# Kernel optimization log

Hardware: AMD Instinct MI355X
Metric: run time of the kernel (lower is better)

Reference implementation:

```python
import jax, jax.numpy as jnp
import numpy as np

N = 1024       # sentence length (words incl. root at index 0)
WD = 300       # word embedding dim (GloVe-style)
PD = 25        # pos_emb_dim
H = 125        # hidden_dim_lstm
FC = 100       # hidden_dim_fc
PVOCAB = 50    # POS tagset size


def setup_inputs() -> dict:
    key = jax.random.key(0)
    ks = jax.random.split(key, 14)
    f = lambda k, s: jax.random.normal(k, s, dtype=jnp.float32) * 0.1
    d_in = WD + PD
    return {
        "word_vecs": jax.random.normal(ks[0], (N, WD), dtype=jnp.float32),
        "pos_idx": jax.random.randint(ks[1], (N,), 0, PVOCAB),
        "parents_ids": jax.random.randint(ks[2], (N,), 0, N),
        "pos_emb": f(ks[3], (PVOCAB, PD)),
        "Wih0": f(ks[4], (2, 4 * H, d_in)),
        "Whh0": f(ks[5], (2, 4 * H, H)),
        "b0": f(ks[6], (2, 4 * H)),
        "Wih1": f(ks[7], (2, 4 * H, 2 * H)),
        "Whh1": f(ks[8], (2, 4 * H, H)),
        "b1": f(ks[9], (2, 4 * H)),
        "fc1_W": f(ks[10], (FC, 4 * H)),
        "fc1_b": f(ks[11], (FC,)),
        "fc2_W": f(ks[12], (1, FC)),
        "fc2_b": f(ks[13], (1,)),
    }


def _lstm_dir(x, Wih, Whh, b, reverse):
    # torch LSTM cell, gate order (i, f, g, o); b = b_ih + b_hh
    Hd = Whh.shape[1]
    def step(carry, xt):
        h, c = carry
        g = xt @ Wih.T + h @ Whh.T + b
        i, fg, gg, o = jnp.split(g, 4)
        i = jax.nn.sigmoid(i)
        fg = jax.nn.sigmoid(fg)
        gg = jnp.tanh(gg)
        o = jax.nn.sigmoid(o)
        c = fg * c + i * gg
        h = o * jnp.tanh(c)
        return (h, c), h
    init = (jnp.zeros((Hd,), x.dtype), jnp.zeros((Hd,), x.dtype))
    _, hs = jax.lax.scan(step, init, x, reverse=reverse)
    return hs  # [n, H], already in original time order


def _bilstm_layer(x, Wih, Whh, b):
    hf = _lstm_dir(x, Wih[0], Whh[0], b[0], False)
    hb = _lstm_dir(x, Wih[1], Whh[1], b[1], True)
    return jnp.concatenate([hf, hb], axis=1)  # [n, 2H]


def reference(word_vecs, pos_idx, parents_ids, pos_emb, Wih0, Whh0, b0,
              Wih1, Whh1, b1, fc1_W, fc1_b, fc2_W, fc2_b):
    # encoder: concat word + pos embeddings, 2-layer BiLSTM
    x = jnp.concatenate([word_vecs, pos_emb[pos_idx]], axis=1)  # [n, WD+PD]
    h = _bilstm_layer(x, Wih0, Whh0, b0)
    h = _bilstm_layer(h, Wih1, Whh1, b1)  # [n, 2H]
    n = h.shape[0]
    twoH = h.shape[1]
    # fc1(cat(h_i, h_j)) = h_i @ W_head^T + h_j @ W_child^T + b  (vectorized over all pairs)
    A = h @ fc1_W[:, :twoH].T   # head contribution  [n, FC]
    B = h @ fc1_W[:, twoH:].T   # child contribution [n, FC]
    T = jnp.tanh(A[:, None, :] + B[None, :, :] + fc1_b)  # [n, n, FC]
    raw = T @ fc2_W[0] + fc2_b[0]                         # [n, n]
    ii = jnp.arange(n)
    # original loop skips diagonal and arcs into the root (j == 0); those stay 0
    mask = (ii[:, None] != ii[None, :]) & (ii[None, :] != 0)
    scores_mat = jnp.where(mask, raw, jnp.float32(0.0))
    logits = scores_mat.T  # row j = scores of heads for child j
    logp = jax.nn.log_softmax(logits, axis=1)
    loss = -jnp.mean(logp[jnp.arange(n), parents_ids])
    return loss, scores_mat
```

## Files before the change

kernel.cpp:

```cpp
#include <hip/hip_runtime.h>

typedef float v2f __attribute__((ext_vector_type(2)));
typedef float v4f __attribute__((ext_vector_type(4)));

#define LOG2E 1.4426950408889634f
#define LN2   0.6931471805599453f

__device__ __forceinline__ float fexp2(float x) {
  float r; asm("v_exp_f32 %0, %1" : "=v"(r) : "v"(x)); return r;
}
__device__ __forceinline__ float frcp(float x) {
  float r; asm("v_rcp_f32 %0, %1" : "=v"(r) : "v"(x)); return r;
}
__device__ __forceinline__ float flog2(float x) {
  float r; asm("v_log_f32 %0, %1" : "=v"(r) : "v"(x)); return r;
}
__device__ __forceinline__ v2f pkfma(v2f a, v2f b, v2f c) {
  v2f d; asm("v_pk_fma_f32 %0, %1, %2, %3" : "=v"(d) : "v"(a), "v"(b), "v"(c));
  return d;
}
__device__ __forceinline__ float dpp_xor1(float v) {
  return __builtin_bit_cast(float,
      __builtin_amdgcn_update_dpp(0, __builtin_bit_cast(int, v), 0xB1, 0xF, 0xF, true));
}
__device__ __forceinline__ float dpp_xor2(float v) {
  return __builtin_bit_cast(float,
      __builtin_amdgcn_update_dpp(0, __builtin_bit_cast(int, v), 0x4E, 0xF, 0xF, true));
}
__device__ __forceinline__ void barrier_lgkm() {
  asm volatile("s_waitcnt lgkmcnt(0)\n\ts_barrier" ::: "memory");
}

__global__ void k_embed(const float* __restrict__ wv, const int* __restrict__ pidx,
                        const float* __restrict__ pemb, float* __restrict__ X) {
  int t = blockIdx.x;
  int pi = pidx[t];
  for (int c = threadIdx.x; c < 336; c += 128) {
    float v;
    if (c < 300)      v = wv[t * 300 + c];
    else if (c < 325) v = pemb[pi * 25 + (c - 300)];
    else              v = 0.f;
    X[t * 336 + c] = v;
  }
}

__global__ void k_repack(const float* __restrict__ src, float* __restrict__ dst,
                         int sK, int dK, int doScale) {
  int r = blockIdx.x;
  float sc = 1.f;
  if (doScale) { int gate = (r % 500) / 125; sc = (gate == 2) ? 2.f * LOG2E : LOG2E; }
  for (int c = threadIdx.x; c < dK; c += 128)
    dst[r * dK + c] = (c < sK) ? src[r * sK + c] * sc : 0.f;
}

__global__ void k_bscale(const float* __restrict__ b, float* __restrict__ bs) {
  int i = blockIdx.x * 256 + threadIdx.x;
  if (i < 1000) {
    int gate = (i % 500) / 125;
    bs[i] = b[i] * ((gate == 2) ? 2.f * LOG2E : LOG2E);
  }
}

__global__ void k_wab(const float* __restrict__ fc1W, float* __restrict__ Wab) {
  int r = blockIdx.x;
  int sr = (r < 100) ? r : r - 100;
  int so = (r < 100) ? 0 : 250;
  for (int c = threadIdx.x; c < 256; c += 128)
    Wab[r * 256 + c] = (c < 250) ? fc1W[sr * 500 + so + c] : 0.f;
}

__global__ void k_misc(const float* __restrict__ fc1b, const float* __restrict__ fc2W,
                       float* __restrict__ biasAB, float* __restrict__ sumw) {
  __shared__ float red[128];
  int t = threadIdx.x;
  for (int c = t; c < 256; c += 128)
    biasAB[c] = (c < 100) ? fc1b[c] : 0.f;
  float s = (t < 100) ? fc2W[t] : 0.f;
  red[t] = s; __syncthreads();
  for (int off = 64; off; off >>= 1) {
    if (t < off) red[t] += red[t + off];
    __syncthreads();
  }
  if (t == 0) sumw[0] = red[0];
}

#define BM 64
#define BN 64
#define BKK 16
__global__ __launch_bounds__(256) void k_gemm(
    const float* __restrict__ A, const float* __restrict__ Bw,
    const float* __restrict__ bias, float* __restrict__ C,
    int M, int N, int K, int ldC, long sBz, long sCz, long sbz, int transOut) {
  const int z = blockIdx.z;
  const float* Bp = Bw + (size_t)z * sBz;
  const float* bp = bias + (size_t)z * sbz;
  float* Cp = C + (size_t)z * sCz;
  const int bm = blockIdx.y * BM, bn = blockIdx.x * BN;
  __shared__ __align__(16) float As[BKK][BM + 4];
  __shared__ __align__(16) float Bs[BKK][BN + 4];
  __shared__ float Ts[BN][BM + 1];
  const int tid = threadIdx.x;
  const int tx = tid & 15, ty = tid >> 4;
  const int lr = tid >> 2;
  const int lk = (tid & 3) * 4;
  float acc[4][4];
#pragma unroll
  for (int a = 0; a < 4; ++a)
#pragma unroll
    for (int b = 0; b < 4; ++b) acc[a][b] = 0.f;

  int brow = bn + lr; if (brow >= N) brow = N - 1;
  for (int k0 = 0; k0 < K; k0 += BKK) {
    float4 a4 = *(const float4*)(A + (size_t)(bm + lr) * K + k0 + lk);
    float4 b4 = *(const float4*)(Bp + (size_t)brow * K + k0 + lk);
    __syncthreads();
    As[lk + 0][lr] = a4.x; As[lk + 1][lr] = a4.y; As[lk + 2][lr] = a4.z; As[lk + 3][lr] = a4.w;
    Bs[lk + 0][lr] = b4.x; Bs[lk + 1][lr] = b4.y; Bs[lk + 2][lr] = b4.z; Bs[lk + 3][lr] = b4.w;
    __syncthreads();
#pragma unroll
    for (int kk = 0; kk < BKK; ++kk) {
      float4 av = *(const float4*)&As[kk][ty * 4];
      float4 bv = *(const float4*)&Bs[kk][tx * 4];
      float aa[4] = {av.x, av.y, av.z, av.w};
      float bb[4] = {bv.x, bv.y, bv.z, bv.w};
#pragma unroll
      for (int a = 0; a < 4; ++a)
#pragma unroll
        for (int b = 0; b < 4; ++b)
          acc[a][b] = __builtin_fmaf(aa[a], bb[b], acc[a][b]);
    }
  }
  if (!transOut) {
#pragma unroll
    for (int a = 0; a < 4; ++a) {
      int i = bm + ty * 4 + a;
#pragma unroll
      for (int b = 0; b < 4; ++b) {
        int j = bn + tx * 4 + b;
        if (j < N) Cp[(size_t)i * ldC + j] = acc[a][b] + bp[j];
      }
    }
  } else {
    __syncthreads();
#pragma unroll
    for (int a = 0; a < 4; ++a)
#pragma unroll
      for (int b = 0; b < 4; ++b) {
        int jn = bn + tx * 4 + b; if (jn >= N) jn = N - 1;
        Ts[tx * 4 + b][ty * 4 + a] = acc[a][b] + bp[jn];
      }
    __syncthreads();
    const int n2 = tid >> 2, mq = (tid & 3) * 16;
    const int n = bn + n2;
    if (n < N) {
#pragma unroll
      for (int r = 0; r < 4; ++r) {
        int m0 = mq + r * 4;
        float4 v;
        v.x = Ts[n2][m0 + 0]; v.y = Ts[n2][m0 + 1];
        v.z = Ts[n2][m0 + 2]; v.w = Ts[n2][m0 + 3];
        *(float4*)(Cp + (size_t)n * ldC + bm + m0) = v;
      }
    }
  }
}

template<bool FWD>
__device__ __forceinline__ void rec_loop(
    const float4* __restrict__ Pr, const v2f (&w)[4][16],
    float (*hb)[160], float (*hist)[128],
    float* __restrict__ hout, int d, int t, int u, int sub, bool active,
    float sA, float sB) {
  const bool b1s = (sub & 1) != 0;
  const bool b2s = (sub & 2) != 0;
  const bool wr = (sub == 0) && active;
  float cst = 0.f;
  float4 cura = Pr[FWD ? 0 : 254];
  float4 curb = Pr[FWD ? 1 : 255];
  barrier_lgkm();

  for (int cb = 0; cb < 128; ++cb) {
    int nc = (cb + 1 < 128) ? cb + 1 : cb;
    float4 nxta = Pr[FWD ? 2 * nc     : 254 - 2 * nc];
    float4 nxtb = Pr[FWD ? 2 * nc + 1 : 255 - 2 * nc];
#pragma unroll
    for (int e = 0; e < 8; ++e) {
      const int buf = e & 1;
      float pre;
      if (FWD)
        pre = (e == 0) ? cura.x : (e == 1) ? cura.y : (e == 2) ? cura.z : (e == 3) ? cura.w
            : (e == 4) ? curb.x : (e == 5) ? curb.y : (e == 6) ? curb.z : curb.w;
      else
        pre = (e == 0) ? curb.w : (e == 1) ? curb.z : (e == 2) ? curb.y : (e == 3) ? curb.x
            : (e == 4) ? cura.w : (e == 5) ? cura.z : (e == 6) ? cura.y : cura.x;
      const v4f* hp = (const v4f*)&hb[buf][36 * sub];
      v2f a0 = {0.f, 0.f}, a1 = {0.f, 0.f}, a2 = {0.f, 0.f}, a3 = {0.f, 0.f};
#pragma unroll
      for (int q = 0; q < 8; ++q) {
        v4f hv = hp[q];
        v2f ha = __builtin_shufflevector(hv, hv, 0, 1);
        v2f hc = __builtin_shufflevector(hv, hv, 2, 3);
        a0 = pkfma(w[0][2 * q], ha, a0); a0 = pkfma(w[0][2 * q + 1], hc, a0);
        a1 = pkfma(w[1][2 * q], ha, a1); a1 = pkfma(w[1][2 * q + 1], hc, a1);
        a2 = pkfma(w[2][2 * q], ha, a2); a2 = pkfma(w[2][2 * q + 1], hc, a2);
        a3 = pkfma(w[3][2 * q], ha, a3); a3 = pkfma(w[3][2 * q + 1], hc, a3);
      }
      float p0 = a0.x + a0.y, p1 = a1.x + a1.y, p2 = a2.x + a2.y, p3 = a3.x + a3.y;
      float s01 = b1s ? p0 : p1, k01 = b1s ? p1 : p0;
      float r01 = k01 + dpp_xor1(s01);
      float s23 = b1s ? p2 : p3, k23 = b1s ? p3 : p2;
      float r23 = k23 + dpp_xor1(s23);
      float sv = b2s ? r01 : r23, kv = b2s ? r23 : r01;
      float x = kv + dpp_xor2(sv) + pre;
      float sg = frcp(1.f + fexp2(-x));
      float a = __builtin_fmaf(sA, sg, sB);
      float fg = dpp_xor1(a);
      float gg = dpp_xor2(a);
      float og = dpp_xor2(fg);
      cst = __builtin_fmaf(fg, cst, a * gg);
      float th = __builtin_fmaf(2.f, frcp(1.f + fexp2(-2.f * LOG2E * cst)), -1.f);
      float h = og * th;
      if (wr) {
        hb[buf ^ 1][u + 4 * (u >> 5)] = h;
        hist[(cb & 3) * 8 + e][u] = h;
      }
      barrier_lgkm();
    }
    if ((cb & 3) == 3) {
      const int S0 = (cb - 3) * 8;
#pragma unroll
      for (int k = 0; k < 8; ++k) {
        int idx = t + k * 512;
        int r = idx >> 7, u2 = idx & 127;
        if (u2 < 125) {
          int step = S0 + r;
          int time = FWD ? step : 1023 - step;
          hout[(size_t)time * 256 + d * 125 + u2] = hist[r][u2];
        }
      }
      barrier_lgkm();
    }
    cura = nxta; curb = nxtb;
  }
}

__global__ __launch_bounds__(512, 2) void k_rec(const float* __restrict__ Pt,
                                                const float* __restrict__ Whh,
                                                float* __restrict__ hout) {
  const int d = blockIdx.x;
  const int t = threadIdx.x;
  int u = t >> 2; const bool active = (u < 125); if (u > 124) u = 124;
  const int sub = t & 3;

  const float* Wd = Whh + (size_t)d * 500 * 125;
  v2f w[4][16];
#pragma unroll
  for (int g = 0; g < 4; ++g) {
    const float sc = (g == 2) ? 2.f * LOG2E : LOG2E;
    const float* wrp = Wd + (size_t)(g * 125 + u) * 125;
#pragma unroll
    for (int j = 0; j < 16; ++j) {
      int col = sub * 32 + 2 * j;
      v2f ww;
      ww.x = (col     < 125) ? wrp[col]     * sc : 0.f;
      ww.y = (col + 1 < 125) ? wrp[col + 1] * sc : 0.f;
      w[g][j] = ww;
    }
  }

  __shared__ __align__(16) float hb[2][160];
  __shared__ float hist[32][128];
  for (int i = t; i < 320; i += 512) ((float*)hb)[i] = 0.f;

  const int prow = sub * 125 + u;
  const float4* Pr = (const float4*)(Pt + (size_t)d * 500 * 1024 + (size_t)prow * 1024);
  const float sA = (sub == 2) ? 2.f : 1.f;
  const float sB = (sub == 2) ? -1.f : 0.f;

  if (d == 0) rec_loop<true >(Pr, w, hb, hist, hout, d, t, u, sub, active, sA, sB);
  else        rec_loop<false>(Pr, w, hb, hist, hout, d, t, u, sub, active, sA, sB);
}

__global__ __launch_bounds__(256) void k_pair(const float* __restrict__ AB,
    const float* __restrict__ fc2W, const float* __restrict__ fc2b,
    const float* __restrict__ sumw, float* __restrict__ outS,
    float* __restrict__ scoresT) {
  __shared__ float As[32][100];
  __shared__ float Bs[32][101];
  __shared__ float w2s[100];
  const int tid = threadIdx.x;
  const int i0 = blockIdx.y * 32, j0 = blockIdx.x * 32;
  for (int idx = tid; idx < 3200; idx += 256) {
    int r = idx / 100, k = idx - r * 100;
    As[r][k] = AB[(size_t)(i0 + r) * 200 + k];
    Bs[r][k] = AB[(size_t)(j0 + r) * 200 + 100 + k];
  }
  if (tid < 100) w2s[tid] = 2.f * fc2W[tid];
  __syncthreads();
  const int tx = tid & 31, ty = tid >> 5;
  float acc[4] = {0.f, 0.f, 0.f, 0.f};
#pragma unroll 4
  for (int k = 0; k < 100; ++k) {
    float b = Bs[tx][k];
    float wk2 = w2s[k];
    float bs = b * (2.f * LOG2E);
#pragma unroll
    for (int q = 0; q < 4; ++q) {
      float a = As[ty + 8 * q][k];
      float r = frcp(1.f + fexp2(__builtin_fmaf(a, 2.f * LOG2E, bs)));
      acc[q] = __builtin_fmaf(wk2, r, acc[q]);
    }
  }
  float base = sumw[0] + fc2b[0];
  const int j = j0 + tx;
#pragma unroll
  for (int q = 0; q < 4; ++q) {
    int i = i0 + ty + 8 * q;
    float val = (i != j && j != 0) ? (base - acc[q]) : 0.f;
    outS[(size_t)i * 1024 + j] = val;
    scoresT[(size_t)j * 1024 + i] = val;
  }
}

__global__ __launch_bounds__(256) void k_soft(const float* __restrict__ scoresT,
    const int* __restrict__ parents, float* __restrict__ contrib) {
  const int j = blockIdx.x, tid = threadIdx.x;
  __shared__ float red[256];
  const float* row = scoresT + (size_t)j * 1024;
  float v0 = row[tid], v1 = row[tid + 256], v2 = row[tid + 512], v3 = row[tid + 768];
  float m = fmaxf(fmaxf(v0, v1), fmaxf(v2, v3));
  red[tid] = m; __syncthreads();
  for (int off = 128; off; off >>= 1) {
    if (tid < off) red[tid] = fmaxf(red[tid], red[tid + off]);
    __syncthreads();
  }
  m = red[0]; __syncthreads();
  float s = fexp2((v0 - m) * LOG2E) + fexp2((v1 - m) * LOG2E) +
            fexp2((v2 - m) * LOG2E) + fexp2((v3 - m) * LOG2E);
  red[tid] = s; __syncthreads();
  for (int off = 128; off; off >>= 1) {
    if (tid < off) red[tid] += red[tid + off];
    __syncthreads();
  }
  if (tid == 0) {
    float S = red[0];
    int p = parents[j];
    contrib[j] = row[p] - m - flog2(S) * LN2;
  }
}

__global__ __launch_bounds__(256) void k_loss(const float* __restrict__ contrib,
                                              float* __restrict__ out) {
  __shared__ float red[256];
  int tid = threadIdx.x;
  float s = contrib[tid] + contrib[tid + 256] + contrib[tid + 512] + contrib[tid + 768];
  red[tid] = s; __syncthreads();
  for (int off = 128; off; off >>= 1) {
    if (tid < off) red[tid] += red[tid + off];
    __syncthreads();
  }
  if (tid == 0) out[0] = -red[0] * (1.f / 1024.f);
}

extern "C" void kernel_launch(void* const* d_in, const int* in_sizes, int n_in,
                              void* d_out, int out_size, void* d_ws, size_t ws_size,
                              hipStream_t stream) {
  const float* wv   = (const float*)d_in[0];
  const int*   pidx = (const int*)d_in[1];
  const int*   par  = (const int*)d_in[2];
  const float* pemb = (const float*)d_in[3];
  const float* Wih0 = (const float*)d_in[4];
  const float* Whh0 = (const float*)d_in[5];
  const float* b0   = (const float*)d_in[6];
  const float* Wih1 = (const float*)d_in[7];
  const float* Whh1 = (const float*)d_in[8];
  const float* b1   = (const float*)d_in[9];
  const float* fc1W = (const float*)d_in[10];
  const float* fc1b = (const float*)d_in[11];
  const float* fc2W = (const float*)d_in[12];
  const float* fc2b = (const float*)d_in[13];
  float* ws = (float*)d_ws;
  float* X      = ws + 0;
  float* Wih0p  = ws + 344064;
  float* Pt0    = ws + 680064;
  float* h0     = ws + 1704064;
  float* Wih1p  = ws + 1966208;
  float* Pt1    = ws + 2222208;
  float* h1     = ws + 3246208;
  float* Wab    = ws + 3508352;
  float* biasAB = ws + 3559552;
  float* AB     = ws + 3559808;
  float* scT    = ws + 3764608;
  float* contrib= ws + 4813184;
  float* sumw   = ws + 4814208;
  float* bs0    = ws + 4814212;
  float* bs1    = ws + 4815212;
  float* out = (float*)d_out;

  hipMemsetAsync(h0, 0, 1024 * 256 * sizeof(float), stream);
  hipMemsetAsync(h1, 0, 1024 * 256 * sizeof(float), stream);

  k_embed <<<1024, 128, 0, stream>>>(wv, pidx, pemb, X);
  k_repack<<<1000, 128, 0, stream>>>(Wih0, Wih0p, 325, 336, 1);
  k_repack<<<1000, 128, 0, stream>>>(Wih1, Wih1p, 250, 256, 1);
  k_bscale<<<4, 256, 0, stream>>>(b0, bs0);
  k_bscale<<<4, 256, 0, stream>>>(b1, bs1);
  k_wab   <<<200, 128, 0, stream>>>(fc1W, Wab);
  k_misc  <<<1, 128, 0, stream>>>(fc1b, fc2W, biasAB, sumw);

  k_gemm<<<dim3(8, 16, 2), 256, 0, stream>>>(X, Wih0p, bs0, Pt0, 1024, 500, 336, 1024,
                                             500L * 336, 500L * 1024, 500L, 1);
  k_rec <<<2, 512, 0, stream>>>(Pt0, Whh0, h0);
  k_gemm<<<dim3(8, 16, 2), 256, 0, stream>>>(h0, Wih1p, bs1, Pt1, 1024, 500, 256, 1024,
                                             500L * 256, 500L * 1024, 500L, 1);
  k_rec <<<2, 512, 0, stream>>>(Pt1, Whh1, h1);
  k_gemm<<<dim3(4, 16, 1), 256, 0, stream>>>(h1, Wab, biasAB, AB, 1024, 200, 256, 200,
                                             0L, 0L, 0L, 0);
  k_pair<<<dim3(32, 32), 256, 0, stream>>>(AB, fc2W, fc2b, sumw, out + 1, scT);
  k_soft<<<1024, 256, 0, stream>>>(scT, par, contrib);
  k_loss<<<1, 256, 0, stream>>>(contrib, out);
}
```

Measured before the change: 1.354 ms.

## Restructure LSTM recurrence to 2 threads per unit computing all four gates

The recurrent kernel now assigns each hidden unit to 2 lanes instead of 4. Each lane covers half of the hidden vector for all four gates, which replaces the gate-transposing DPP shuffles with a single xor1 reduction per gate. The input-projection scale is halved (the two lanes each add half of it), and the block shrinks to 256 threads, which removes one reduction level and the cross-lane gate exchange on the serial critical path. In exchange each lane does twice the FMAs and holds 256 weight registers, so register pressure and per-step compute latency go up.

```diff
diff --git a/kernel.cpp b/kernel.cpp
--- a/kernel.cpp
+++ b/kernel.cpp
@@ -15,17 +15,12 @@
 __device__ __forceinline__ float flog2(float x) {
   float r; asm("v_log_f32 %0, %1" : "=v"(r) : "v"(x)); return r;
 }
-__device__ __forceinline__ v2f pkfma(v2f a, v2f b, v2f c) {
-  v2f d; asm("v_pk_fma_f32 %0, %1, %2, %3" : "=v"(d) : "v"(a), "v"(b), "v"(c));
-  return d;
+__device__ __forceinline__ void pkfma(v2f& c, v2f a, v2f b) {
+  asm("v_pk_fma_f32 %0, %1, %2, %0" : "+v"(c) : "v"(a), "v"(b));
 }
 __device__ __forceinline__ float dpp_xor1(float v) {
   return __builtin_bit_cast(float,
       __builtin_amdgcn_update_dpp(0, __builtin_bit_cast(int, v), 0xB1, 0xF, 0xF, true));
-}
-__device__ __forceinline__ float dpp_xor2(float v) {
-  return __builtin_bit_cast(float,
-      __builtin_amdgcn_update_dpp(0, __builtin_bit_cast(int, v), 0x4E, 0xF, 0xF, true));
 }
 __device__ __forceinline__ void barrier_lgkm() {
   asm volatile("s_waitcnt lgkmcnt(0)\n\ts_barrier" ::: "memory");
@@ -48,7 +43,7 @@
                          int sK, int dK, int doScale) {
   int r = blockIdx.x;
   float sc = 1.f;
-  if (doScale) { int gate = (r % 500) / 125; sc = (gate == 2) ? 2.f * LOG2E : LOG2E; }
+  if (doScale) { int gate = (r % 500) / 125; sc = (gate == 2) ? LOG2E : 0.5f * LOG2E; }
   for (int c = threadIdx.x; c < dK; c += 128)
     dst[r * dK + c] = (c < sK) ? src[r * sK + c] * sc : 0.f;
 }
@@ -57,7 +52,7 @@
   int i = blockIdx.x * 256 + threadIdx.x;
   if (i < 1000) {
     int gate = (i % 500) / 125;
-    bs[i] = b[i] * ((gate == 2) ? 2.f * LOG2E : LOG2E);
+    bs[i] = b[i] * ((gate == 2) ? LOG2E : 0.5f * LOG2E);
   }
 }
 
@@ -165,72 +160,65 @@
   }
 }
 
+__device__ __forceinline__ float elem(float4 v, int e) {
+  return (e == 0) ? v.x : (e == 1) ? v.y : (e == 2) ? v.z : v.w;
+}
+
 template<bool FWD>
 __device__ __forceinline__ void rec_loop(
-    const float4* __restrict__ Pr, const v2f (&w)[4][16],
-    float (*hb)[160], float (*hist)[128],
-    float* __restrict__ hout, int d, int t, int u, int sub, bool active,
-    float sA, float sB) {
-  const bool b1s = (sub & 1) != 0;
-  const bool b2s = (sub & 2) != 0;
-  const bool wr = (sub == 0) && active;
+    const float4* __restrict__ P0, const float4* __restrict__ P1,
+    const float4* __restrict__ P2, const float4* __restrict__ P3,
+    const v2f (&w)[4][32], float (*hb)[128], float (*hist)[128],
+    float* __restrict__ hout, int d, int t, int u, int sub, bool wr) {
   float cst = 0.f;
-  float4 cura = Pr[FWD ? 0 : 254];
-  float4 curb = Pr[FWD ? 1 : 255];
+  float4 cur0 = P0[FWD ? 0 : 255], cur1 = P1[FWD ? 0 : 255];
+  float4 cur2 = P2[FWD ? 0 : 255], cur3 = P3[FWD ? 0 : 255];
   barrier_lgkm();
 
-  for (int cb = 0; cb < 128; ++cb) {
-    int nc = (cb + 1 < 128) ? cb + 1 : cb;
-    float4 nxta = Pr[FWD ? 2 * nc     : 254 - 2 * nc];
-    float4 nxtb = Pr[FWD ? 2 * nc + 1 : 255 - 2 * nc];
-#pragma unroll
-    for (int e = 0; e < 8; ++e) {
+  for (int cb = 0; cb < 256; ++cb) {
+    int nc = (cb + 1 < 256) ? cb + 1 : cb;
+    int ni = FWD ? nc : 255 - nc;
+    float4 nxt0 = P0[ni], nxt1 = P1[ni], nxt2 = P2[ni], nxt3 = P3[ni];
+#pragma unroll
+    for (int e = 0; e < 4; ++e) {
       const int buf = e & 1;
-      float pre;
-      if (FWD)
-        pre = (e == 0) ? cura.x : (e == 1) ? cura.y : (e == 2) ? cura.z : (e == 3) ? cura.w
-            : (e == 4) ? curb.x : (e == 5) ? curb.y : (e == 6) ? curb.z : curb.w;
-      else
-        pre = (e == 0) ? curb.w : (e == 1) ? curb.z : (e == 2) ? curb.y : (e == 3) ? curb.x
-            : (e == 4) ? cura.w : (e == 5) ? cura.z : (e == 6) ? cura.y : cura.x;
-      const v4f* hp = (const v4f*)&hb[buf][36 * sub];
+      const int ee = FWD ? e : 3 - e;
+      float pr0 = elem(cur0, ee), pr1 = elem(cur1, ee);
+      float pr2 = elem(cur2, ee), pr3 = elem(cur3, ee);
+      const v4f* hp = (const v4f*)&hb[buf][sub * 64];
       v2f a0 = {0.f, 0.f}, a1 = {0.f, 0.f}, a2 = {0.f, 0.f}, a3 = {0.f, 0.f};
 #pragma unroll
-      for (int q = 0; q < 8; ++q) {
+      for (int q = 0; q < 16; ++q) {
         v4f hv = hp[q];
         v2f ha = __builtin_shufflevector(hv, hv, 0, 1);
         v2f hc = __builtin_shufflevector(hv, hv, 2, 3);
-        a0 = pkfma(w[0][2 * q], ha, a0); a0 = pkfma(w[0][2 * q + 1], hc, a0);
-        a1 = pkfma(w[1][2 * q], ha, a1); a1 = pkfma(w[1][2 * q + 1], hc, a1);
-        a2 = pkfma(w[2][2 * q], ha, a2); a2 = pkfma(w[2][2 * q + 1], hc, a2);
-        a3 = pkfma(w[3][2 * q], ha, a3); a3 = pkfma(w[3][2 * q + 1], hc, a3);
-      }
-      float p0 = a0.x + a0.y, p1 = a1.x + a1.y, p2 = a2.x + a2.y, p3 = a3.x + a3.y;
-      float s01 = b1s ? p0 : p1, k01 = b1s ? p1 : p0;
-      float r01 = k01 + dpp_xor1(s01);
-      float s23 = b1s ? p2 : p3, k23 = b1s ? p3 : p2;
-      float r23 = k23 + dpp_xor1(s23);
-      float sv = b2s ? r01 : r23, kv = b2s ? r23 : r01;
-      float x = kv + dpp_xor2(sv) + pre;
-      float sg = frcp(1.f + fexp2(-x));
-      float a = __builtin_fmaf(sA, sg, sB);
-      float fg = dpp_xor1(a);
-      float gg = dpp_xor2(a);
-      float og = dpp_xor2(fg);
-      cst = __builtin_fmaf(fg, cst, a * gg);
+        pkfma(a0, w[0][2 * q], ha); pkfma(a0, w[0][2 * q + 1], hc);
+        pkfma(a1, w[1][2 * q], ha); pkfma(a1, w[1][2 * q + 1], hc);
+        pkfma(a2, w[2][2 * q], ha); pkfma(a2, w[2][2 * q + 1], hc);
+        pkfma(a3, w[3][2 * q], ha); pkfma(a3, w[3][2 * q + 1], hc);
+      }
+      float p0 = a0.x + a0.y + pr0;  p0 += dpp_xor1(p0);
+      float p1 = a1.x + a1.y + pr1;  p1 += dpp_xor1(p1);
+      float p2 = a2.x + a2.y + pr2;  p2 += dpp_xor1(p2);
+      float p3 = a3.x + a3.y + pr3;  p3 += dpp_xor1(p3);
+      float gi = frcp(1.f + fexp2(-p0));
+      float gf = frcp(1.f + fexp2(-p1));
+      float gg = __builtin_fmaf(2.f, frcp(1.f + fexp2(-p2)), -1.f);
+      float go = frcp(1.f + fexp2(-p3));
+      cst = __builtin_fmaf(gf, cst, gi * gg);
       float th = __builtin_fmaf(2.f, frcp(1.f + fexp2(-2.f * LOG2E * cst)), -1.f);
-      float h = og * th;
+      float h = go * th;
       if (wr) {
-        hb[buf ^ 1][u + 4 * (u >> 5)] = h;
-        hist[(cb & 3) * 8 + e][u] = h;
+        hb[buf ^ 1][u] = h;
+        hist[(cb & 7) * 4 + e][u] = h;
       }
       barrier_lgkm();
     }
-    if ((cb & 3) == 3) {
-      const int S0 = (cb - 3) * 8;
-#pragma unroll
-      for (int k = 0; k < 8; ++k) {
-        int idx = t + k * 512;
+    if ((cb & 7) == 7) {
+      const int S0 = 4 * cb - 28;
+#pragma unroll
+      for (int k = 0; k < 16; ++k) {
+        int idx = t + k * 256;
         int r = idx >> 7, u2 = idx & 127;
         if (u2 < 125) {
           int step = S0 + r;
@@ -240,27 +228,28 @@
       }
       barrier_lgkm();
     }
-    cura = nxta; curb = nxtb;
-  }
-}
-
-__global__ __launch_bounds__(512, 2) void k_rec(const float* __restrict__ Pt,
+    cur0 = nxt0; cur1 = nxt1; cur2 = nxt2; cur3 = nxt3;
+  }
+}
+
+__global__ __launch_bounds__(256, 1) void k_rec(const float* __restrict__ Pt,
                                                 const float* __restrict__ Whh,
                                                 float* __restrict__ hout) {
   const int d = blockIdx.x;
   const int t = threadIdx.x;
-  int u = t >> 2; const bool active = (u < 125); if (u > 124) u = 124;
-  const int sub = t & 3;
+  int u = t >> 1; const bool active = (u < 125); if (u > 124) u = 124;
+  const int sub = t & 1;
+  const bool wr = (sub == 0) && active;
 
   const float* Wd = Whh + (size_t)d * 500 * 125;
-  v2f w[4][16];
+  v2f w[4][32];
 #pragma unroll
   for (int g = 0; g < 4; ++g) {
     const float sc = (g == 2) ? 2.f * LOG2E : LOG2E;
     const float* wrp = Wd + (size_t)(g * 125 + u) * 125;
 #pragma unroll
-    for (int j = 0; j < 16; ++j) {
-      int col = sub * 32 + 2 * j;
+    for (int j = 0; j < 32; ++j) {
+      int col = sub * 64 + 2 * j;
       v2f ww;
       ww.x = (col     < 125) ? wrp[col]     * sc : 0.f;
       ww.y = (col + 1 < 125) ? wrp[col + 1] * sc : 0.f;
@@ -268,17 +257,18 @@
     }
   }
 
-  __shared__ __align__(16) float hb[2][160];
+  __shared__ __align__(16) float hb[2][128];
   __shared__ float hist[32][128];
-  for (int i = t; i < 320; i += 512) ((float*)hb)[i] = 0.f;
-
-  const int prow = sub * 125 + u;
-  const float4* Pr = (const float4*)(Pt + (size_t)d * 500 * 1024 + (size_t)prow * 1024);
-  const float sA = (sub == 2) ? 2.f : 1.f;
-  const float sB = (sub == 2) ? -1.f : 0.f;
-
-  if (d == 0) rec_loop<true >(Pr, w, hb, hist, hout, d, t, u, sub, active, sA, sB);
-  else        rec_loop<false>(Pr, w, hb, hist, hout, d, t, u, sub, active, sA, sB);
+  ((float*)hb)[t] = 0.f;
+
+  const float4* Pb = (const float4*)(Pt + (size_t)d * 500 * 1024);
+  const float4* P0 = Pb + (size_t)(0 * 125 + u) * 256;
+  const float4* P1 = Pb + (size_t)(1 * 125 + u) * 256;
+  const float4* P2 = Pb + (size_t)(2 * 125 + u) * 256;
+  const float4* P3 = Pb + (size_t)(3 * 125 + u) * 256;
+
+  if (d == 0) rec_loop<true >(P0, P1, P2, P3, w, hb, hist, hout, d, t, u, sub, wr);
+  else        rec_loop<false>(P0, P1, P2, P3, w, hb, hist, hout, d, t, u, sub, wr);
 }
 
 __global__ __launch_bounds__(256) void k_pair(const float* __restrict__ AB,
@@ -410,10 +400,10 @@
 
   k_gemm<<<dim3(8, 16, 2), 256, 0, stream>>>(X, Wih0p, bs0, Pt0, 1024, 500, 336, 1024,
                                              500L * 336, 500L * 1024, 500L, 1);
-  k_rec <<<2, 512, 0, stream>>>(Pt0, Whh0, h0);
+  k_rec <<<2, 256, 0, stream>>>(Pt0, Whh0, h0);
   k_gemm<<<dim3(8, 16, 2), 256, 0, stream>>>(h0, Wih1p, bs1, Pt1, 1024, 500, 256, 1024,
                                              500L * 256, 500L * 1024, 500L, 1);
-  k_rec <<<2, 512, 0, stream>>>(Pt1, Whh1, h1);
+  k_rec <<<2, 256, 0, stream>>>(Pt1, Whh1, h1);
   k_gemm<<<dim3(4, 16, 1), 256, 0, stream>>>(h1, Wab, biasAB, AB, 1024, 200, 256, 200,
                                              0L, 0L, 0L, 0);
   k_pair<<<dim3(32, 32), 256, 0, stream>>>(AB, fc2W, fc2b, sumw, out + 1, scT);
```

Result: slower. 2.229 ms (+64.6%).
